# Kernel tuning notes

Hardware: AMD Instinct MI355X
Metric: run time of the kernel (lower is better)

## Reference

```python
import jax, jax.numpy as jnp
import numpy as np

V, D, H, KVH, HD, I, L, T_MAX, THETA = 32000, 1024, 16, 4, 64, 2816, 2, 2048, 10000.0
EPS = 1e-5


def rmsnorm(x, w):
    return x * jax.lax.rsqrt(jnp.mean(x * x, axis=-1, keepdims=True) + EPS) * w


def rope_cos_sin(T):
    inv = 1.0 / (THETA ** (jnp.arange(0, HD, 2, dtype=jnp.float32) / HD))  # [HD/2]
    ang = jnp.arange(T, dtype=jnp.float32)[:, None] * inv[None, :]         # [T, HD/2]
    return jnp.cos(ang), jnp.sin(ang)


def apply_rope(x, cos, sin):
    # x: [B, T, h, HD]; interleaved complex pairs as in torch.view_as_complex
    x0 = x[..., 0::2]
    x1 = x[..., 1::2]
    c = cos[None, :, None, :]
    s = sin[None, :, None, :]
    o0 = x0 * c - x1 * s
    o1 = x0 * s + x1 * c
    return jnp.stack([o0, o1], axis=-1).reshape(x.shape)


def setup_inputs() -> dict:
    key = jax.random.key(0)
    ks = jax.random.split(key, 12)
    sc = 0.02
    return {
        "toks": jax.random.randint(ks[0], (1, 2048), 0, V),
        "embed": jax.random.normal(ks[1], (V, D), jnp.float32) * sc,
        "Wq": jax.random.normal(ks[2], (L, D, H * HD), jnp.float32) * sc,
        "Wk": jax.random.normal(ks[3], (L, D, KVH * HD), jnp.float32) * sc,
        "Wv": jax.random.normal(ks[4], (L, D, KVH * HD), jnp.float32) * sc,
        "Wo": jax.random.normal(ks[5], (L, H * HD, D), jnp.float32) * sc,
        "Wgate": jax.random.normal(ks[6], (L, D, I), jnp.float32) * sc,
        "Wup": jax.random.normal(ks[7], (L, D, I), jnp.float32) * sc,
        "Wdown": jax.random.normal(ks[8], (L, I, D), jnp.float32) * sc,
        "ln1_w": jnp.ones((L, D), jnp.float32),
        "ln2_w": jnp.ones((L, D), jnp.float32),
        "norm_w": jnp.ones((D,), jnp.float32),
        "Wlm": jax.random.normal(ks[9], (D, V), jnp.float32) * sc,
    }


def reference(toks, embed, Wq, Wk, Wv, Wo, Wgate, Wup, Wdown, ln1_w, ln2_w, norm_w, Wlm):
    B, T = toks.shape
    cos, sin = rope_cos_sin(T)
    causal = jnp.tril(jnp.ones((T, T), dtype=bool))
    add_mask = jnp.where(causal, 0.0, -jnp.inf).astype(jnp.float32)  # [T, T]
    n_rep = H // KVH
    scale = 1.0 / np.sqrt(HD)

    x = embed[toks]  # [B, T, D]
    for l in range(L):
        h = rmsnorm(x, ln1_w[l])
        q = (h @ Wq[l]).reshape(B, T, H, HD)
        k = (h @ Wk[l]).reshape(B, T, KVH, HD)
        v = (h @ Wv[l]).reshape(B, T, KVH, HD)
        q = apply_rope(q, cos, sin)
        k = apply_rope(k, cos, sin)
        k = jnp.repeat(k, n_rep, axis=2)  # GQA repeat_kv -> [B, T, H, HD]
        v = jnp.repeat(v, n_rep, axis=2)
        # materialized scores [B, H, T, T] (faithful to source)
        scores = jnp.einsum('bqhd,bkhd->bhqk', q, k) * scale + add_mask[None, None]
        probs = jax.nn.softmax(scores, axis=-1)
        attn = jnp.einsum('bhqk,bkhd->bqhd', probs, v).reshape(B, T, H * HD)
        x = x + attn @ Wo[l]
        h = rmsnorm(x, ln2_w[l])
        x = x + (jax.nn.silu(h @ Wgate[l]) * (h @ Wup[l])) @ Wdown[l]

    x = rmsnorm(x, norm_w)
    return x @ Wlm  # [B, T, V]
```

## Files before the change

kernel.cpp:

```cpp
#include <hip/hip_runtime.h>

#define T_SEQ 2048
#define DMODEL 1024
#define NH 16
#define NKV 4
#define HEAD_DIM 64
#define FFDIM 2816
#define NVOCAB 32000

#define QBLK 64
#define KBLK 128
#define KSS 72
#define VTS 136
#define PSS 136

using u16 = unsigned short;
typedef __bf16 bf16x8 __attribute__((ext_vector_type(8)));
typedef float f32x4 __attribute__((ext_vector_type(4)));

__device__ __forceinline__ float b2f(u16 u) {
    union { unsigned int i; float f; } v; v.i = ((unsigned int)u) << 16; return v.f;
}
__device__ __forceinline__ u16 f2b(float f) {
    unsigned int u = __builtin_bit_cast(unsigned int, f);
    unsigned int r = (u + 0x7FFFu + ((u >> 16) & 1u)) >> 16;
    return (u16)r;
}
__device__ __forceinline__ void gload16(const u16* g, u16* l) {
    __builtin_amdgcn_global_load_lds(
        (const __attribute__((address_space(1))) void*)g,
        (__attribute__((address_space(3))) void*)l, 16, 0, 0);
}

__global__ __launch_bounds__(256) void embed_rms_kernel(const int* __restrict__ toks,
                                                        const float* __restrict__ emb,
                                                        const float* __restrict__ w,
                                                        float* __restrict__ x,
                                                        u16* __restrict__ h) {
    __shared__ float red[256];
    const int row = blockIdx.x, tid = threadIdx.x;
    const float* er = emb + (size_t)toks[row] * DMODEL;
    float vals[4]; float ss = 0.f;
#pragma unroll
    for (int i = 0; i < 4; i++) {
        float v = er[tid + 256 * i];
        vals[i] = v; ss += v * v;
        x[(size_t)row * DMODEL + tid + 256 * i] = v;
    }
    red[tid] = ss; __syncthreads();
    for (int s = 128; s > 0; s >>= 1) { if (tid < s) red[tid] += red[tid + s]; __syncthreads(); }
    float inv = rsqrtf(red[0] * (1.0f / DMODEL) + 1e-5f);
#pragma unroll
    for (int i = 0; i < 4; i++) {
        int c = tid + 256 * i;
        h[(size_t)row * DMODEL + c] = f2b(vals[i] * inv * w[c]);
    }
}

__global__ __launch_bounds__(256) void rmsnorm_kernel(const float* __restrict__ x,
                                                      const float* __restrict__ w,
                                                      u16* __restrict__ out) {
    __shared__ float red[256];
    const int row = blockIdx.x, tid = threadIdx.x;
    const float* xr = x + (size_t)row * DMODEL;
    float vals[4]; float ss = 0.f;
#pragma unroll
    for (int i = 0; i < 4; i++) { float v = xr[tid + 256 * i]; vals[i] = v; ss += v * v; }
    red[tid] = ss; __syncthreads();
    for (int s = 128; s > 0; s >>= 1) { if (tid < s) red[tid] += red[tid + s]; __syncthreads(); }
    float inv = rsqrtf(red[0] * (1.0f / DMODEL) + 1e-5f);
#pragma unroll
    for (int i = 0; i < 4; i++) {
        int c = tid + 256 * i;
        out[(size_t)row * DMODEL + c] = f2b(vals[i] * inv * w[c]);
    }
}

__global__ __launch_bounds__(256) void tcast_kernel(const float* __restrict__ in,
                                                    u16* __restrict__ out, int K, int N,
                                                    size_t in_ls, size_t out_ls) {
    __shared__ float tile[32][33];
    in += (size_t)blockIdx.z * in_ls;
    out += (size_t)blockIdx.z * out_ls;
    int bx = blockIdx.x * 32;
    int by = blockIdx.y * 32;
    int tx = threadIdx.x & 31, ty = threadIdx.x >> 5;
#pragma unroll
    for (int i = 0; i < 32; i += 8)
        tile[ty + i][tx] = in[(size_t)(by + ty + i) * N + bx + tx];
    __syncthreads();
#pragma unroll
    for (int i = 0; i < 32; i += 8)
        out[(size_t)(bx + ty + i) * K + by + tx] = f2b(tile[tx][ty + i]);
}

__global__ __launch_bounds__(256) void ropeall_kernel(const u16* __restrict__ fqkv,
                                                      u16* __restrict__ qb,
                                                      u16* __restrict__ kb,
                                                      u16* __restrict__ vt) {
    __shared__ u16 tile[32][33];
    const int bid = blockIdx.x, tid = threadIdx.x;
    if (bid < 5120) {
        int heads, coloff, idx;
        u16* out;
        if (bid < 4096) { heads = NH; coloff = 0; out = qb; idx = bid * 256 + tid; }
        else            { heads = NKV; coloff = 1024; out = kb; idx = (bid - 4096) * 256 + tid; }
        int i = idx & 31;
        int rest = idx >> 5;
        int t = rest / heads, hh = rest - t * heads;
        float inv = expf(-(float)i * (9.210340371976184f / 32.0f));
        float ang = (float)t * inv;
        float c = cosf(ang), s = sinf(ang);
        size_t src = (size_t)t * 1536 + coloff + hh * HEAD_DIM + 2 * i;
        size_t dst = (size_t)rest * HEAD_DIM + 2 * i;
        float x0 = b2f(fqkv[src]), x1 = b2f(fqkv[src + 1]);
        out[dst]     = f2b(x0 * c - x1 * s);
        out[dst + 1] = f2b(x0 * s + x1 * c);
    } else {
        int b2 = bid - 5120;
        int bx = (b2 & 7) * 32;
        int by = (b2 >> 3) * 32;
        int tx = tid & 31, ty = tid >> 5;
#pragma unroll
        for (int i = 0; i < 32; i += 8)
            tile[ty + i][tx] = fqkv[(size_t)(by + ty + i) * 1536 + 1280 + bx + tx];
        __syncthreads();
#pragma unroll
        for (int i = 0; i < 32; i += 8)
            vt[(size_t)(bx + ty + i) * T_SEQ + by + tx] = tile[tx][ty + i];
    }
}

template<bool OUT_BF16, bool ADD>
__global__ __launch_bounds__(256) void gemm_bt_kernel(const u16* __restrict__ A,
                                                      const u16* __restrict__ BT,
                                                      void* __restrict__ Cp,
                                                      int N, int K) {
    __shared__ __align__(16) u16 As[2][128 * 32];
    __shared__ __align__(16) u16 Bs[2][128 * 32];
    const int tid = threadIdx.x;
    const int gx = gridDim.x;
    const int nwg = gx * gridDim.y;
    const int hwid = blockIdx.y * gx + blockIdx.x;
    const int q = nwg >> 3, r = nwg & 7;
    const int xcd = hwid & 7, rem = hwid >> 3;
    const int wgid = (xcd < r ? xcd * (q + 1) : r * (q + 1) + (xcd - r) * q) + rem;
    const int brow = wgid % gx, bcol = wgid / gx;

    const int w = tid >> 6, lane = tid & 63;
    const int wr = w >> 1, wc = w & 1;
    const int lg = lane >> 4, lr = lane & 15;

    f32x4 acc[4][4] = {};

    const int srow = w * 32 + (lane >> 2);
    const int scol = (lane & 3) << 3;
    const u16* gA = A + (size_t)(brow * 128 + srow) * K + scol;
    const u16* gB = BT + (size_t)(bcol * 128 + srow) * K + scol;
    const size_t koff16 = (size_t)16 * K;
    const int lofs0 = (w * 32) * 32;
    const int lofs1 = (w * 32 + 16) * 32;

    const int nt = K >> 5;
    gload16(gA, &As[0][lofs0]);
    gload16(gA + koff16, &As[0][lofs1]);
    gload16(gB, &Bs[0][lofs0]);
    gload16(gB + koff16, &Bs[0][lofs1]);
    __syncthreads();

    int cur = 0;
    for (int t = 0; t < nt; t++) {
        if (t + 1 < nt) {
            const int kb = (t + 1) << 5;
            gload16(gA + kb, &As[cur ^ 1][lofs0]);
            gload16(gA + koff16 + kb, &As[cur ^ 1][lofs1]);
            gload16(gB + kb, &Bs[cur ^ 1][lofs0]);
            gload16(gB + koff16 + kb, &Bs[cur ^ 1][lofs1]);
        }
        bf16x8 aF[4], bF[4];
#pragma unroll
        for (int m = 0; m < 4; m++)
            aF[m] = *(const bf16x8*)(&As[cur][(wr * 64 + m * 16 + lr) * 32 + lg * 8]);
#pragma unroll
        for (int n = 0; n < 4; n++)
            bF[n] = *(const bf16x8*)(&Bs[cur][(wc * 64 + n * 16 + lr) * 32 + lg * 8]);
#pragma unroll
        for (int m = 0; m < 4; m++)
#pragma unroll
            for (int n = 0; n < 4; n++)
                acc[m][n] = __builtin_amdgcn_mfma_f32_16x16x32_bf16(aF[m], bF[n], acc[m][n], 0, 0, 0);
        __syncthreads();
        cur ^= 1;
    }

#pragma unroll
    for (int m = 0; m < 4; m++)
#pragma unroll
        for (int n = 0; n < 4; n++)
#pragma unroll
            for (int j = 0; j < 4; j++) {
                int row = brow * 128 + wr * 64 + m * 16 + lg * 4 + j;
                int col = bcol * 128 + wc * 64 + n * 16 + lr;
                size_t idx = (size_t)row * N + col;
                float v = acc[m][n][j];
                if constexpr (OUT_BF16) {
                    ((u16*)Cp)[idx] = f2b(v);
                } else if constexpr (ADD) {
                    ((float*)Cp)[idx] = ((const float*)Cp)[idx] + v;
                } else {
                    ((float*)Cp)[idx] = v;
                }
            }
}

__global__ __launch_bounds__(512) void gemm256_kernel(const u16* __restrict__ A,
                                                      const u16* __restrict__ BT,
                                                      float* __restrict__ C,
                                                      int N, int K) {
    extern __shared__ __align__(16) u16 lds[];
    const int tid = threadIdx.x;
    const int gx = gridDim.x;
    const int nwg = gx * gridDim.y;
    const int hwid = blockIdx.y * gx + blockIdx.x;
    const int q = nwg >> 3, r = nwg & 7;
    const int xcd = hwid & 7, rem = hwid >> 3;
    const int wgid = (xcd < r ? xcd * (q + 1) : r * (q + 1) + (xcd - r) * q) + rem;
    const int bR = wgid % gx, bC = wgid / gx;

    const int w = tid >> 6, lane = tid & 63;
    const int wm = w >> 2, wn = w & 3;
    const int lg = lane >> 4, lr = lane & 15;

    f32x4 acc[8][4] = {};

    const int srow = lane >> 2;
    const int scol = ((lane & 3) ^ ((lane >= 32) ? 2 : 0)) << 3;
    const int rblk = (((lr >= 8) ? (lg ^ 2) : lg)) << 4;

    const u16* Ab = A + (size_t)(bR * 256) * K + scol;
    const u16* Bb = BT + (size_t)(bC * 256) * K + scol;

    auto STAGE_A = [&](int t, int b) {
        gload16(Ab + (size_t)(w * 16 + srow) * K + t * 32,
                lds + (b * 16384 + w * 1024) / 2);
        gload16(Ab + (size_t)((w + 8) * 16 + srow) * K + t * 32,
                lds + (b * 16384 + (w + 8) * 1024) / 2);
    };
    auto STAGE_B = [&](int t, int b) {
        gload16(Bb + (size_t)(w * 16 + srow) * K + t * 32,
                lds + (49152 + b * 16384 + w * 1024) / 2);
        gload16(Bb + (size_t)((w + 8) * 16 + srow) * K + t * 32,
                lds + (49152 + b * 16384 + (w + 8) * 1024) / 2);
    };

    const int nt = K >> 5;
    STAGE_A(0, 0); STAGE_B(0, 0);
    STAGE_A(1, 1); STAGE_B(1, 1);
    asm volatile("s_waitcnt vmcnt(4)" ::: "memory");
    __builtin_amdgcn_s_barrier();

    int cur = 0;
    for (int t = 0; t < nt; t++) {
        const bool st = (t + 2 < nt);
        const int nb = (cur >= 1) ? cur - 1 : cur + 2;
        bf16x8 bF[4];
        {
            bf16x8 aF[4];
#pragma unroll
            for (int mi = 0; mi < 4; mi++)
                aF[mi] = *(const bf16x8*)((const char*)lds + cur * 16384 +
                                          (wm * 8 + mi) * 1024 + lr * 64 + rblk);
#pragma unroll
            for (int n = 0; n < 4; n++)
                bF[n] = *(const bf16x8*)((const char*)lds + 49152 + cur * 16384 +
                                         (wn * 4 + n) * 1024 + lr * 64 + rblk);
            if (st) STAGE_A(t + 2, nb);
            __builtin_amdgcn_s_barrier();
            asm volatile("s_waitcnt lgkmcnt(0)" ::: "memory");
            __builtin_amdgcn_sched_barrier(0);
            __builtin_amdgcn_s_setprio(1);
#pragma unroll
            for (int mi = 0; mi < 4; mi++)
#pragma unroll
                for (int n = 0; n < 4; n++)
                    acc[mi][n] = __builtin_amdgcn_mfma_f32_16x16x32_bf16(
                        aF[mi], bF[n], acc[mi][n], 0, 0, 0);
            __builtin_amdgcn_s_setprio(0);
            __builtin_amdgcn_s_barrier();
        }
        {
            bf16x8 aF[4];
#pragma unroll
            for (int mi = 0; mi < 4; mi++)
                aF[mi] = *(const bf16x8*)((const char*)lds + cur * 16384 +
                                          (wm * 8 + 4 + mi) * 1024 + lr * 64 + rblk);
            if (st) STAGE_B(t + 2, nb);
            if (t + 1 < nt) {
                if (st) asm volatile("s_waitcnt vmcnt(4)" ::: "memory");
                else    asm volatile("s_waitcnt vmcnt(0)" ::: "memory");
            }
            __builtin_amdgcn_s_barrier();
            asm volatile("s_waitcnt lgkmcnt(0)" ::: "memory");
            __builtin_amdgcn_sched_barrier(0);
            __builtin_amdgcn_s_setprio(1);
#pragma unroll
            for (int mi = 0; mi < 4; mi++)
#pragma unroll
                for (int n = 0; n < 4; n++)
                    acc[4 + mi][n] = __builtin_amdgcn_mfma_f32_16x16x32_bf16(
                        aF[mi], bF[n], acc[4 + mi][n], 0, 0, 0);
            __builtin_amdgcn_s_setprio(0);
            __builtin_amdgcn_s_barrier();
        }
        cur = (cur == 2) ? 0 : cur + 1;
    }

#pragma unroll
    for (int m = 0; m < 8; m++)
#pragma unroll
        for (int n = 0; n < 4; n++)
#pragma unroll
            for (int jj = 0; jj < 4; jj++) {
                int row = bR * 256 + wm * 128 + m * 16 + lg * 4 + jj;
                int col = bC * 256 + wn * 64 + n * 16 + lr;
                C[(size_t)row * N + col] = acc[m][n][jj];
            }
}

__device__ __forceinline__ int bs_off(int c, int k) {
    return c * 40 + ((((k >> 3) ^ ((c >> 3) & 3)) << 3) | (k & 7));
}

__global__ __launch_bounds__(256) void gemm_f32b_kernel(const u16* __restrict__ A,
                                                        const float* __restrict__ B,
                                                        float* __restrict__ C,
                                                        int N, int K) {
    __shared__ __align__(16) u16 As[128 * 40];
    __shared__ __align__(16) u16 Bs[128 * 40];
    const int tid = threadIdx.x;
    const int brow = blockIdx.y, bcol = blockIdx.x;
    const int wid = tid >> 6, lane = tid & 63;
    const int wr = wid >> 1, wc = wid & 1;
    const int lg = lane >> 4, lr = lane & 15;

    f32x4 acc[4][4] = {};
    const int ar = tid >> 2, ac = (tid & 3) << 3;
    const int bk = tid >> 4, bc = (tid & 15) << 3;

    for (int kb = 0; kb < K; kb += 32) {
        {
            const u16* ga = A + (size_t)(brow * 128 + ar) * K + kb + ac;
            *(uint4*)(&As[ar * 40 + ac]) = *(const uint4*)ga;
            *(uint4*)(&As[(ar + 64) * 40 + ac]) = *(const uint4*)(ga + (size_t)64 * K);
        }
        {
            const float* gb = B + (size_t)(kb + bk) * N + bcol * 128 + bc;
            float4 a0 = *(const float4*)gb;
            float4 a1 = *(const float4*)(gb + 4);
            float4 b0 = *(const float4*)(gb + (size_t)16 * N);
            float4 b1 = *(const float4*)(gb + (size_t)16 * N + 4);
            float f0[8] = {a0.x, a0.y, a0.z, a0.w, a1.x, a1.y, a1.z, a1.w};
            float f1[8] = {b0.x, b0.y, b0.z, b0.w, b1.x, b1.y, b1.z, b1.w};
#pragma unroll
            for (int i = 0; i < 8; i++) {
                Bs[bs_off(bc + i, bk)] = f2b(f0[i]);
                Bs[bs_off(bc + i, bk + 16)] = f2b(f1[i]);
            }
        }
        __syncthreads();

        bf16x8 aF[4], bF[4];
#pragma unroll
        for (int m = 0; m < 4; m++)
            aF[m] = *(const bf16x8*)(&As[(wr * 64 + m * 16 + lr) * 40 + lg * 8]);
#pragma unroll
        for (int n = 0; n < 4; n++) {
            int c = wc * 64 + n * 16 + lr;
            bF[n] = *(const bf16x8*)(&Bs[c * 40 + ((lg ^ ((c >> 3) & 3)) << 3)]);
        }
#pragma unroll
        for (int m = 0; m < 4; m++)
#pragma unroll
            for (int n = 0; n < 4; n++)
                acc[m][n] = __builtin_amdgcn_mfma_f32_16x16x32_bf16(aF[m], bF[n], acc[m][n], 0, 0, 0);
        __syncthreads();
    }

#pragma unroll
    for (int m = 0; m < 4; m++)
#pragma unroll
        for (int n = 0; n < 4; n++)
#pragma unroll
            for (int j = 0; j < 4; j++) {
                int row = brow * 128 + wr * 64 + m * 16 + lg * 4 + j;
                int col = bcol * 128 + wc * 64 + n * 16 + lr;
                C[(size_t)row * N + col] = acc[m][n][j];
            }
}

__global__ __launch_bounds__(256) void fattn_kernel(const u16* __restrict__ q,
                                                    const u16* __restrict__ k,
                                                    const u16* __restrict__ vt,
                                                    u16* __restrict__ out) {
    __shared__ __align__(16) u16 Ks[KBLK * KSS];
    __shared__ __align__(16) u16 Vt[HEAD_DIM * VTS];
    __shared__ __align__(16) u16 Ps[QBLK * PSS];
    const int tid = threadIdx.x;
    const int qb0 = blockIdx.x * QBLK, h = blockIdx.y, kvh = h >> 2;
    const int w = tid >> 6, lane = tid & 63;
    const int lg = lane >> 4, lr = lane & 15;

    bf16x8 qf0, qf1;
    {
        const u16* src = q + ((size_t)(qb0 + w * 16 + lr) * NH + h) * HEAD_DIM;
        qf0 = *(const bf16x8*)(src + lg * 8);
        qf1 = *(const bf16x8*)(src + 32 + lg * 8);
    }

    f32x4 acc_o[4] = {};
    float m_run[4] = {-1e30f, -1e30f, -1e30f, -1e30f};
    float l_run[4] = {0.f, 0.f, 0.f, 0.f};

    const int ntiles = (qb0 + QBLK - 1) / KBLK + 1;

    for (int kt = 0; kt < ntiles; kt++) {
        const int kb = kt * KBLK;
        __syncthreads();
        for (int c = tid; c < KBLK * 8; c += 256) {
            int row = c >> 3, c8 = (c & 7) << 3;
            *(uint4*)(&Ks[row * KSS + c8]) =
                *(const uint4*)(k + ((size_t)(kb + row) * NKV + kvh) * HEAD_DIM + c8);
        }
        for (int c = tid; c < HEAD_DIM * 16; c += 256) {
            int d = c >> 4, c16 = (c & 15) << 3;
            *(uint4*)(&Vt[d * VTS + c16]) =
                *(const uint4*)(vt + (size_t)(kvh * HEAD_DIM + d) * T_SEQ + kb + c16);
        }
        __syncthreads();

        f32x4 s[8] = {};
#pragma unroll
        for (int n = 0; n < 8; n++) {
            bf16x8 kf0 = *(const bf16x8*)(&Ks[(n * 16 + lr) * KSS + lg * 8]);
            bf16x8 kf1 = *(const bf16x8*)(&Ks[(n * 16 + lr) * KSS + 32 + lg * 8]);
            s[n] = __builtin_amdgcn_mfma_f32_16x16x32_bf16(qf0, kf0, s[n], 0, 0, 0);
            s[n] = __builtin_amdgcn_mfma_f32_16x16x32_bf16(qf1, kf1, s[n], 0, 0, 0);
        }

#pragma unroll
        for (int j = 0; j < 4; j++) {
            int q_g = qb0 + w * 16 + lg * 4 + j;
            float sv[8];
            float tmax = -1e30f;
#pragma unroll
            for (int n = 0; n < 8; n++) {
                float xx = s[n][j] * 0.125f;
                if (kb + n * 16 + lr > q_g) xx = -1e30f;
                sv[n] = xx;
                tmax = fmaxf(tmax, xx);
            }
#pragma unroll
            for (int mm = 1; mm < 16; mm <<= 1) tmax = fmaxf(tmax, __shfl_xor(tmax, mm));
            float mn = fmaxf(m_run[j], tmax);
            float sc = __expf(m_run[j] - mn);
            m_run[j] = mn;
            float rsum = 0.f;
#pragma unroll
            for (int n = 0; n < 8; n++) {
                float p = __expf(sv[n] - mn);
                rsum += p;
                Ps[(w * 16 + lg * 4 + j) * PSS + n * 16 + lr] = f2b(p);
            }
#pragma unroll
            for (int mm = 1; mm < 16; mm <<= 1) rsum += __shfl_xor(rsum, mm);
            l_run[j] = l_run[j] * sc + rsum;
#pragma unroll
            for (int n = 0; n < 4; n++) acc_o[n][j] *= sc;
        }

#pragma unroll
        for (int ks = 0; ks < 4; ks++) {
            bf16x8 pf = *(const bf16x8*)(&Ps[(w * 16 + lr) * PSS + ks * 32 + lg * 8]);
#pragma unroll
            for (int n = 0; n < 4; n++) {
                bf16x8 vf = *(const bf16x8*)(&Vt[(n * 16 + lr) * VTS + ks * 32 + lg * 8]);
                acc_o[n] = __builtin_amdgcn_mfma_f32_16x16x32_bf16(pf, vf, acc_o[n], 0, 0, 0);
            }
        }
    }

#pragma unroll
    for (int n = 0; n < 4; n++)
#pragma unroll
        for (int j = 0; j < 4; j++) {
            int t = qb0 + w * 16 + lg * 4 + j;
            int d = n * 16 + lr;
            out[((size_t)t * NH + h) * HEAD_DIM + d] = f2b(acc_o[n][j] / l_run[j]);
        }
}

__global__ __launch_bounds__(256) void silu_mul_kernel(const u16* __restrict__ gu,
                                                       u16* __restrict__ out) {
    int t = blockIdx.x;
    int c = blockIdx.y * 256 + threadIdx.x;
    float gv = b2f(gu[(size_t)t * 5632 + c]);
    float uv = b2f(gu[(size_t)t * 5632 + 2816 + c]);
    float s = gv / (1.f + __expf(-gv));
    out[(size_t)t * FFDIM + c] = f2b(s * uv);
}

extern "C" void kernel_launch(void* const* d_in, const int* in_sizes, int n_in,
                              void* d_out, int out_size, void* d_ws, size_t ws_size,
                              hipStream_t stream) {
    const int*   toks = (const int*)d_in[0];
    const float* emb  = (const float*)d_in[1];
    const float* Wq   = (const float*)d_in[2];
    const float* Wk   = (const float*)d_in[3];
    const float* Wv   = (const float*)d_in[4];
    const float* Wo   = (const float*)d_in[5];
    const float* Wg   = (const float*)d_in[6];
    const float* Wu   = (const float*)d_in[7];
    const float* Wd   = (const float*)d_in[8];
    const float* ln1  = (const float*)d_in[9];
    const float* ln2  = (const float*)d_in[10];
    const float* nw   = (const float*)d_in[11];
    const float* Wlm  = (const float*)d_in[12];

    char* ob = (char*)d_out;
    const size_t MB = 1024 * 1024;
    float* x    = (float*)(ob + 0 * MB);
    u16* fqkv   = (u16*)  (ob + 8 * MB);
    u16* fGU    = (u16*)  (ob + 16 * MB);
    u16* vt     = (u16*)  (ob + 40 * MB);
    u16* qb     = (u16*)  (ob + 42 * MB);
    u16* kb     = (u16*)  (ob + 47 * MB);
    u16* attnb  = (u16*)  (ob + 48 * MB);
    u16* ffb    = (u16*)  (ob + 52 * MB);
    u16* Wt = (u16*)(ob + 64 * MB);
    const size_t OFF_QKV = 0;
    const size_t OFF_O   = (size_t)1536 * 1024;
    const size_t OFF_GU  = OFF_O + (size_t)1024 * 1024;
    const size_t OFF_D   = OFF_GU + (size_t)5632 * 1024;
    const size_t LS      = OFF_D + (size_t)2816 * 1024;
    u16* h = (u16*)d_ws;
    bool ws_big = ws_size >= 72 * MB;
    u16* WlmT = ws_big ? (u16*)((char*)d_ws + 4 * MB) : nullptr;
    (void)in_sizes; (void)n_in; (void)out_size;

    dim3 blk(256);
    auto tc = [&](const float* in, u16* out, int K, int N, size_t in_ls, int nz) {
        tcast_kernel<<<dim3(N / 32, K / 32, nz), blk, 0, stream>>>(in, out, K, N, in_ls, LS);
    };
    auto gemm_f32 = [&](const u16* A, const u16* BT, float* C, int N, int K, bool add) {
        dim3 g(T_SEQ / 128, N / 128);
        if (add) gemm_bt_kernel<false, true><<<g, blk, 0, stream>>>(A, BT, (void*)C, N, K);
        else     gemm_bt_kernel<false, false><<<g, blk, 0, stream>>>(A, BT, (void*)C, N, K);
    };
    auto gemm_b16 = [&](const u16* A, const u16* BT, u16* C, int N, int K) {
        dim3 g(T_SEQ / 128, N / 128);
        gemm_bt_kernel<true, false><<<g, blk, 0, stream>>>(A, BT, (void*)C, N, K);
    };

    tc(Wq, Wt + OFF_QKV,                       DMODEL, NH * HEAD_DIM,  (size_t)DMODEL * NH * HEAD_DIM, 2);
    tc(Wk, Wt + OFF_QKV + (size_t)1024 * 1024, DMODEL, NKV * HEAD_DIM, (size_t)DMODEL * NKV * HEAD_DIM, 2);
    tc(Wv, Wt + OFF_QKV + (size_t)1280 * 1024, DMODEL, NKV * HEAD_DIM, (size_t)DMODEL * NKV * HEAD_DIM, 2);
    tc(Wo, Wt + OFF_O,                         DMODEL, DMODEL,         (size_t)DMODEL * DMODEL, 2);
    tc(Wg, Wt + OFF_GU,                        DMODEL, FFDIM,          (size_t)DMODEL * FFDIM, 2);
    tc(Wu, Wt + OFF_GU + (size_t)FFDIM * 1024, DMODEL, FFDIM,          (size_t)DMODEL * FFDIM, 2);
    tc(Wd, Wt + OFF_D,                         FFDIM,  DMODEL,         (size_t)FFDIM * DMODEL, 2);
    if (WlmT)
        tcast_kernel<<<dim3(NVOCAB / 32, DMODEL / 32, 1), blk, 0, stream>>>(
            Wlm, WlmT, DMODEL, NVOCAB, 0, 0);

    embed_rms_kernel<<<dim3(T_SEQ), blk, 0, stream>>>(toks, emb, ln1, x, h);

    for (int l = 0; l < 2; l++) {
        const u16* WqkvT = Wt + (size_t)l * LS + OFF_QKV;
        const u16* WoT   = Wt + (size_t)l * LS + OFF_O;
        const u16* WguT  = Wt + (size_t)l * LS + OFF_GU;
        const u16* WdT   = Wt + (size_t)l * LS + OFF_D;

        if (l > 0)
            rmsnorm_kernel<<<dim3(T_SEQ), blk, 0, stream>>>(x, ln1 + (size_t)l * DMODEL, h);
        gemm_b16(h, WqkvT, fqkv, 1536, DMODEL);
        ropeall_kernel<<<dim3(5632), blk, 0, stream>>>(fqkv, qb, kb, vt);
        fattn_kernel<<<dim3(T_SEQ / QBLK, NH), blk, 0, stream>>>(qb, kb, vt, attnb);
        gemm_f32(attnb, WoT, x, DMODEL, DMODEL, true);

        rmsnorm_kernel<<<dim3(T_SEQ), blk, 0, stream>>>(x, ln2 + (size_t)l * DMODEL, h);
        gemm_b16(h, WguT, fGU, 5632, DMODEL);
        silu_mul_kernel<<<dim3(T_SEQ, FFDIM / 256), blk, 0, stream>>>(fGU, ffb);
        gemm_f32(ffb, WdT, x, DMODEL, FFDIM, true);
    }

    rmsnorm_kernel<<<dim3(T_SEQ), blk, 0, stream>>>(x, nw, h);
    if (WlmT) {
        (void)hipFuncSetAttribute(reinterpret_cast<const void*>(gemm256_kernel),
                                  hipFuncAttributeMaxDynamicSharedMemorySize, 98304);
        dim3 g(T_SEQ / 256, NVOCAB / 256);
        gemm256_kernel<<<g, dim3(512), 98304, stream>>>(h, WlmT, (float*)d_out,
                                                        NVOCAB, DMODEL);
    } else {
        dim3 g(NVOCAB / 128, T_SEQ / 128);
        gemm_f32b_kernel<<<g, blk, 0, stream>>>(h, Wlm, (float*)d_out, NVOCAB, DMODEL);
    }
}
```

Measured before the change: 812.4 us.

## Fuse SiLU-mul into gate/up GEMM via interleaved weight layout and precompute RoPE table

Gate and up weight columns are interleaved in 16-column groups during the transpose-cast, so the big 256x256 GEMM holds matching gate and up accumulators in the same thread. That GEMM then applies SiLU(g)*u in its epilogue and writes bf16 directly, which removes the intermediate 2048x5632 buffer and the separate silu_mul kernel. RoPE cos/sin values are precomputed once into a table instead of being computed with transcendentals per element, and the head index math uses shifts. The new GEMM path relies on the fragment column mapping matching the 16-wide interleave, and this layout assumption ties the weight transform to the GEMM tiling.

```diff
diff --git a/kernel.cpp b/kernel.cpp
--- a/kernel.cpp
+++ b/kernel.cpp
@@ -94,28 +94,67 @@
         out[(size_t)(bx + ty + i) * K + by + tx] = f2b(tile[tx][ty + i]);
 }
 
+__global__ __launch_bounds__(256) void tcast_gu_kernel(const float* __restrict__ Wg,
+                                                       const float* __restrict__ Wu,
+                                                       u16* __restrict__ out,
+                                                       size_t w_ls, size_t out_ls) {
+    __shared__ float tg[32][17], tu[32][17];
+    Wg += (size_t)blockIdx.z * w_ls;
+    Wu += (size_t)blockIdx.z * w_ls;
+    out += (size_t)blockIdx.z * out_ls;
+    const int Q = blockIdx.x;
+    const int KY = blockIdx.y * 32;
+    const int tid = threadIdx.x;
+    const int tx = tid & 15, ty = tid >> 4;
+#pragma unroll
+    for (int i = 0; i < 32; i += 16) {
+        tg[ty + i][tx] = Wg[(size_t)(KY + ty + i) * FFDIM + Q * 16 + tx];
+        tu[ty + i][tx] = Wu[(size_t)(KY + ty + i) * FFDIM + Q * 16 + tx];
+    }
+    __syncthreads();
+    const int tx2 = tid & 31, ty2 = tid >> 5;
+#pragma unroll
+    for (int i = 0; i < 32; i += 8) {
+        int r = ty2 + i;
+        float v = (r < 16) ? tg[tx2][r] : tu[tx2][r - 16];
+        out[(size_t)(Q * 32 + r) * DMODEL + KY + tx2] = f2b(v);
+    }
+}
+
+__global__ __launch_bounds__(256) void rope_table_kernel(float2* __restrict__ tbl) {
+    int idx = blockIdx.x * 256 + threadIdx.x;
+    int t = idx >> 5, i = idx & 31;
+    float inv = expf(-(float)i * (9.210340371976184f / 32.0f));
+    float ang = (float)t * inv;
+    tbl[idx] = make_float2(cosf(ang), sinf(ang));
+}
+
 __global__ __launch_bounds__(256) void ropeall_kernel(const u16* __restrict__ fqkv,
+                                                      const float2* __restrict__ tbl,
                                                       u16* __restrict__ qb,
                                                       u16* __restrict__ kb,
                                                       u16* __restrict__ vt) {
     __shared__ u16 tile[32][33];
     const int bid = blockIdx.x, tid = threadIdx.x;
     if (bid < 5120) {
-        int heads, coloff, idx;
+        int i, t, hh, coloff;
         u16* out;
-        if (bid < 4096) { heads = NH; coloff = 0; out = qb; idx = bid * 256 + tid; }
-        else            { heads = NKV; coloff = 1024; out = kb; idx = (bid - 4096) * 256 + tid; }
-        int i = idx & 31;
-        int rest = idx >> 5;
-        int t = rest / heads, hh = rest - t * heads;
-        float inv = expf(-(float)i * (9.210340371976184f / 32.0f));
-        float ang = (float)t * inv;
-        float c = cosf(ang), s = sinf(ang);
+        size_t rest;
+        if (bid < 4096) {
+            int idx = bid * 256 + tid;
+            i = idx & 31; rest = idx >> 5;
+            t = (int)(rest >> 4); hh = (int)(rest & 15); coloff = 0; out = qb;
+        } else {
+            int idx = (bid - 4096) * 256 + tid;
+            i = idx & 31; rest = idx >> 5;
+            t = (int)(rest >> 2); hh = (int)(rest & 3); coloff = 1024; out = kb;
+        }
+        float2 cs = tbl[t * 32 + i];
         size_t src = (size_t)t * 1536 + coloff + hh * HEAD_DIM + 2 * i;
-        size_t dst = (size_t)rest * HEAD_DIM + 2 * i;
+        size_t dst = rest * HEAD_DIM + 2 * i;
         float x0 = b2f(fqkv[src]), x1 = b2f(fqkv[src + 1]);
-        out[dst]     = f2b(x0 * c - x1 * s);
-        out[dst + 1] = f2b(x0 * s + x1 * c);
+        out[dst]     = f2b(x0 * cs.x - x1 * cs.y);
+        out[dst + 1] = f2b(x0 * cs.y + x1 * cs.x);
     } else {
         int b2 = bid - 5120;
         int bx = (b2 & 7) * 32;
@@ -213,10 +252,11 @@
             }
 }
 
+template<int MODE>
 __global__ __launch_bounds__(512) void gemm256_kernel(const u16* __restrict__ A,
                                                       const u16* __restrict__ BT,
-                                                      float* __restrict__ C,
-                                                      int N, int K) {
+                                                      void* __restrict__ Cp,
+                                                      int Nout, int K) {
     extern __shared__ __align__(16) u16 lds[];
     const int tid = threadIdx.x;
     const int gx = gridDim.x;
@@ -316,15 +356,29 @@
     }
 
 #pragma unroll
-    for (int m = 0; m < 8; m++)
-#pragma unroll
-        for (int n = 0; n < 4; n++)
-#pragma unroll
-            for (int jj = 0; jj < 4; jj++) {
-                int row = bR * 256 + wm * 128 + m * 16 + lg * 4 + jj;
-                int col = bC * 256 + wn * 64 + n * 16 + lr;
-                C[(size_t)row * N + col] = acc[m][n][jj];
-            }
+    for (int m = 0; m < 8; m++) {
+        if constexpr (MODE == 0) {
+#pragma unroll
+            for (int n = 0; n < 4; n++)
+#pragma unroll
+                for (int jj = 0; jj < 4; jj++) {
+                    int row = bR * 256 + wm * 128 + m * 16 + lg * 4 + jj;
+                    int col = bC * 256 + wn * 64 + n * 16 + lr;
+                    ((float*)Cp)[(size_t)row * Nout + col] = acc[m][n][jj];
+                }
+        } else {
+#pragma unroll
+            for (int n = 0; n < 4; n += 2)
+#pragma unroll
+                for (int jj = 0; jj < 4; jj++) {
+                    int row = bR * 256 + wm * 128 + m * 16 + lg * 4 + jj;
+                    int col = bC * 128 + wn * 32 + (n >> 1) * 16 + lr;
+                    float g = acc[m][n][jj], u = acc[m][n + 1][jj];
+                    float s = g / (1.f + __expf(-g));
+                    ((u16*)Cp)[(size_t)row * Nout + col] = f2b(s * u);
+                }
+        }
+    }
 }
 
 __device__ __forceinline__ int bs_off(int c, int k) {
@@ -497,16 +551,6 @@
             int d = n * 16 + lr;
             out[((size_t)t * NH + h) * HEAD_DIM + d] = f2b(acc_o[n][j] / l_run[j]);
         }
-}
-
-__global__ __launch_bounds__(256) void silu_mul_kernel(const u16* __restrict__ gu,
-                                                       u16* __restrict__ out) {
-    int t = blockIdx.x;
-    int c = blockIdx.y * 256 + threadIdx.x;
-    float gv = b2f(gu[(size_t)t * 5632 + c]);
-    float uv = b2f(gu[(size_t)t * 5632 + 2816 + c]);
-    float s = gv / (1.f + __expf(-gv));
-    out[(size_t)t * FFDIM + c] = f2b(s * uv);
 }
 
 extern "C" void kernel_launch(void* const* d_in, const int* in_sizes, int n_in,
@@ -530,7 +574,7 @@
     const size_t MB = 1024 * 1024;
     float* x    = (float*)(ob + 0 * MB);
     u16* fqkv   = (u16*)  (ob + 8 * MB);
-    u16* fGU    = (u16*)  (ob + 16 * MB);
+    float2* tbl = (float2*)(ob + 16 * MB);
     u16* vt     = (u16*)  (ob + 40 * MB);
     u16* qb     = (u16*)  (ob + 42 * MB);
     u16* kb     = (u16*)  (ob + 47 * MB);
@@ -565,12 +609,18 @@
     tc(Wk, Wt + OFF_QKV + (size_t)1024 * 1024, DMODEL, NKV * HEAD_DIM, (size_t)DMODEL * NKV * HEAD_DIM, 2);
     tc(Wv, Wt + OFF_QKV + (size_t)1280 * 1024, DMODEL, NKV * HEAD_DIM, (size_t)DMODEL * NKV * HEAD_DIM, 2);
     tc(Wo, Wt + OFF_O,                         DMODEL, DMODEL,         (size_t)DMODEL * DMODEL, 2);
-    tc(Wg, Wt + OFF_GU,                        DMODEL, FFDIM,          (size_t)DMODEL * FFDIM, 2);
-    tc(Wu, Wt + OFF_GU + (size_t)FFDIM * 1024, DMODEL, FFDIM,          (size_t)DMODEL * FFDIM, 2);
+    tcast_gu_kernel<<<dim3(FFDIM / 16, DMODEL / 32, 2), blk, 0, stream>>>(
+        Wg, Wu, Wt + OFF_GU, (size_t)DMODEL * FFDIM, LS);
     tc(Wd, Wt + OFF_D,                         FFDIM,  DMODEL,         (size_t)FFDIM * DMODEL, 2);
     if (WlmT)
         tcast_kernel<<<dim3(NVOCAB / 32, DMODEL / 32, 1), blk, 0, stream>>>(
             Wlm, WlmT, DMODEL, NVOCAB, 0, 0);
+    rope_table_kernel<<<dim3(T_SEQ * 32 / 256), blk, 0, stream>>>(tbl);
+
+    (void)hipFuncSetAttribute(reinterpret_cast<const void*>(gemm256_kernel<0>),
+                              hipFuncAttributeMaxDynamicSharedMemorySize, 98304);
+    (void)hipFuncSetAttribute(reinterpret_cast<const void*>(gemm256_kernel<3>),
+                              hipFuncAttributeMaxDynamicSharedMemorySize, 98304);
 
     embed_rms_kernel<<<dim3(T_SEQ), blk, 0, stream>>>(toks, emb, ln1, x, h);
 
@@ -583,23 +633,24 @@
         if (l > 0)
             rmsnorm_kernel<<<dim3(T_SEQ), blk, 0, stream>>>(x, ln1 + (size_t)l * DMODEL, h);
         gemm_b16(h, WqkvT, fqkv, 1536, DMODEL);
-        ropeall_kernel<<<dim3(5632), blk, 0, stream>>>(fqkv, qb, kb, vt);
+        ropeall_kernel<<<dim3(5632), blk, 0, stream>>>(fqkv, tbl, qb, kb, vt);
         fattn_kernel<<<dim3(T_SEQ / QBLK, NH), blk, 0, stream>>>(qb, kb, vt, attnb);
         gemm_f32(attnb, WoT, x, DMODEL, DMODEL, true);
 
         rmsnorm_kernel<<<dim3(T_SEQ), blk, 0, stream>>>(x, ln2 + (size_t)l * DMODEL, h);
-        gemm_b16(h, WguT, fGU, 5632, DMODEL);
-        silu_mul_kernel<<<dim3(T_SEQ, FFDIM / 256), blk, 0, stream>>>(fGU, ffb);
+        {
+            dim3 g(T_SEQ / 256, 5632 / 256);
+            gemm256_kernel<3><<<g, dim3(512), 98304, stream>>>(h, WguT, (void*)ffb,
+                                                               FFDIM, DMODEL);
+        }
         gemm_f32(ffb, WdT, x, DMODEL, FFDIM, true);
     }
 
     rmsnorm_kernel<<<dim3(T_SEQ), blk, 0, stream>>>(x, nw, h);
     if (WlmT) {
-        (void)hipFuncSetAttribute(reinterpret_cast<const void*>(gemm256_kernel),
-                                  hipFuncAttributeMaxDynamicSharedMemorySize, 98304);
         dim3 g(T_SEQ / 256, NVOCAB / 256);
-        gemm256_kernel<<<g, dim3(512), 98304, stream>>>(h, WlmT, (float*)d_out,
-                                                        NVOCAB, DMODEL);
+        gemm256_kernel<0><<<g, dim3(512), 98304, stream>>>(h, WlmT, (void*)d_out,
+                                                           NVOCAB, DMODEL);
     } else {
         dim3 g(NVOCAB / 128, T_SEQ / 128);
         gemm_f32b_kernel<<<g, blk, 0, stream>>>(h, Wlm, (float*)d_out, NVOCAB, DMODEL);
```

New measurement: 799.8 us. Within noise of the previous version (-1.6%).
